# Kernel tuning notes

Hardware: AMD Instinct MI355X
Metric: run time of the kernel (lower is better)

The kernel has to match this reference:

```python
import jax, jax.numpy as jnp
import numpy as np

N, P, C, T, V = 32, 6, 128, 64, 25
S = 3        # num_subset
CI = 32      # inter_channels
EPS = 1e-5
NEG_SLOPE = 0.1


def conv1x1(x, w, b):
    # x: (N,P,Cin,T,V), w: (Cout,Cin), b: (Cout,)
    return jnp.einsum('npctv,oc->npotv', x, w) + b[None, None, :, None, None]


def batchnorm(x, gamma, beta):
    # training-mode BN over (N,P,T,V) per channel, matching torch forward math
    mu = x.mean(axis=(0, 1, 3, 4), keepdims=True)
    var = x.var(axis=(0, 1, 3, 4), keepdims=True)
    xh = (x - mu) * jax.lax.rsqrt(var + EPS)
    return xh * gamma[None, None, :, None, None] + beta[None, None, :, None, None]


def leaky(x):
    return jnp.where(x >= 0, x, NEG_SLOPE * x)


def t_block(inp, att_bias, alphat, w_in, b_in, w_out, b_out, g_out, be_out,
            w_ff, b_ff, g_ff, be_ff):
    n, p, c, t, v = inp.shape
    qk = conv1x1(inp, w_in, b_in)                       # (N,P,2*S*CI,T,V)
    qk = qk.reshape(n, p, 2, S, CI, t, v).transpose(2, 0, 3, 1, 4, 5, 6)
    q, k = qk[0], qk[1]                                 # (N,S,P,CI,T,V)
    scores = jnp.einsum('nspctv,nspcqv->nsptq', q, k) / (CI * v)
    att = att_bias + jnp.tanh(scores) * alphat          # (N,S,P,T,T)
    y = jnp.einsum('npctv,nsptq->nspcqv', inp, att)     # (N,S,P,C,T,V)
    y = y.transpose(0, 2, 1, 3, 4, 5).reshape(n, p, S * c, t, v)
    y = batchnorm(conv1x1(y, w_out, b_out), g_out, be_out)
    y = leaky(inp + y)                                  # residual (identity down path)
    y2 = batchnorm(conv1x1(y, w_ff, b_ff), g_ff, be_ff)
    return leaky(y + y2)


def setup_inputs() -> dict:
    key = jax.random.key(0)
    ks = jax.random.split(key, 8)
    sc = 0.05
    return {
        'x': jax.random.normal(ks[0], (N, P, C, T, V), jnp.float32),
        'att_t1': jnp.zeros((1, S, 1, T, T), jnp.float32),
        'att_t2': jnp.zeros((1, S, 1, T, T), jnp.float32),
        'alphat': jnp.ones((1, S, 1, 1, 1), jnp.float32),
        'w_in': jax.random.normal(ks[1], (2 * S * CI, C), jnp.float32) * sc,
        'b_in': jax.random.normal(ks[2], (2 * S * CI,), jnp.float32) * sc,
        'w_out': jax.random.normal(ks[3], (C, S * C), jnp.float32) * sc,
        'b_out': jax.random.normal(ks[4], (C,), jnp.float32) * sc,
        'g_out': jnp.ones((C,), jnp.float32),
        'be_out': jnp.zeros((C,), jnp.float32),
        'w_ff': jax.random.normal(ks[5], (C, C), jnp.float32) * sc,
        'b_ff': jax.random.normal(ks[6], (C,), jnp.float32) * sc,
        'g_ff': jnp.ones((C,), jnp.float32),
        'be_ff': jnp.zeros((C,), jnp.float32),
    }


def reference(x, att_t1, att_t2, alphat, w_in, b_in, w_out, b_out, g_out,
              be_out, w_ff, b_ff, g_ff, be_ff):
    y = t_block(x, att_t1, alphat, w_in, b_in, w_out, b_out, g_out, be_out,
                w_ff, b_ff, g_ff, be_ff)
    z = t_block(y, att_t2, alphat, w_in, b_in, w_out, b_out, g_out, be_out,
                w_ff, b_ff, g_ff, be_ff)
    return z
```

## Files before the change

kernel.cpp:

```cpp
#include <hip/hip_runtime.h>
#include <hip/hip_bf16.h>
#include <math.h>

#define NPB  192
#define CCH  128
#define TT   64
#define VV   25
#define PIX  1600
#define SS   3
#define EPC  307200.0f
static const size_t ETOT = (size_t)NPB * CCH * PIX;

typedef __attribute__((ext_vector_type(4))) float f32x4;
typedef __attribute__((ext_vector_type(8))) short short8;

__device__ __forceinline__ ushort f2bf(float f) {
    __hip_bfloat16 h = __float2bfloat16(f);
    return __builtin_bit_cast(unsigned short, h);
}
__device__ __forceinline__ float bf2f(ushort u) {
    unsigned int x = ((unsigned int)u) << 16;
    return __builtin_bit_cast(float, x);
}

__global__ void wprep(const float* __restrict__ w_in, const float* __restrict__ b_in,
                      const float* __restrict__ w_out, const float* __restrict__ w_ff,
                      ushort* __restrict__ Wp, float* __restrict__ bp,
                      ushort* __restrict__ Wo, ushort* __restrict__ Wf) {
    int i = blockIdx.x * 256 + threadIdx.x;
    if (i < 192 * 128) {
        int r = i >> 7, c = i & 127;
        int s = r / 64, j = r % 64;
        int src = (j < 32) ? (s * 32 + j) : (96 + s * 32 + (j - 32));
        Wp[i] = f2bf(w_in[src * 128 + c]);
        if (c == 0) bp[r] = b_in[src];
    }
    if (i < 128 * 384) Wo[i] = f2bf(w_out[i]);
    if (i < 128 * 128) Wf[i] = f2bf(w_ff[i]);
}

__global__ void remap_x(const float* __restrict__ x, ushort* __restrict__ xr) {
    size_t o = ((size_t)blockIdx.x * 256 + threadIdx.x) * 4;
    size_t row = o / PIX;
    int p = (int)(o % PIX);
    int v = p >> 6, t0 = p & 63;
    const float* xp = x + row * PIX;
    uint2 u;
    u.x = (uint)f2bf(xp[(t0 + 0) * 25 + v]) | ((uint)f2bf(xp[(t0 + 1) * 25 + v]) << 16);
    u.y = (uint)f2bf(xp[(t0 + 2) * 25 + v]) | ((uint)f2bf(xp[(t0 + 3) * 25 + v]) << 16);
    *(uint2*)(xr + o) = u;
}

__global__ __launch_bounds__(256)
void gemm_conv(const void* __restrict__ inp, int in_bf16,
               const ushort* __restrict__ W, int ldw,
               const float* __restrict__ bias,
               void* __restrict__ outp, int out_bf16, int out_ch,
               int accflag)
{
    __shared__ ushort Wt[64 * 72];
    __shared__ ushort Xt[128 * 72];
    const int np = blockIdx.x;
    const int pixbase = blockIdx.y * 128;
    const int obase = blockIdx.z * 64;
    const int tid = threadIdx.x;
    const int wave = tid >> 6, lane = tid & 63;
    const int quad = lane >> 4, l16 = lane & 15;
    const int wPix = wave * 32;

    f32x4 acc[4][2];
    if (accflag) {
        const float* op = (const float*)outp + ((size_t)np * out_ch + obase) * PIX + pixbase;
#pragma unroll
        for (int ms = 0; ms < 4; ++ms)
#pragma unroll
            for (int ns = 0; ns < 2; ++ns) {
                int pl = wPix + ns * 16 + l16;
                bool valid = (pixbase + pl) < PIX;
#pragma unroll
                for (int r = 0; r < 4; ++r) {
                    int ol = ms * 16 + quad * 4 + r;
                    acc[ms][ns][r] = valid ? op[(size_t)ol * PIX + pl] : 0.f;
                }
            }
    } else {
#pragma unroll
        for (int ms = 0; ms < 4; ++ms) {
            float bv[4];
#pragma unroll
            for (int r = 0; r < 4; ++r) {
                int ol = ms * 16 + quad * 4 + r;
                bv[r] = bias ? bias[obase + ol] : 0.f;
            }
#pragma unroll
            for (int ns = 0; ns < 2; ++ns)
#pragma unroll
                for (int r = 0; r < 4; ++r) acc[ms][ns][r] = bv[r];
        }
    }

    const ushort* inb = (const ushort*)inp;
    const float* inf = (const float*)inp;
    const size_t in_off = (size_t)np * 128 * PIX;

    for (int kc = 0; kc < 2; ++kc) {
        const int kbase = kc * 64;
        {
            int o = tid >> 2, seg = tid & 3;
            const ushort* src = W + (size_t)(obase + o) * ldw + kbase + seg * 16;
            uint4 a = *(const uint4*)src;
            uint4 b = *(const uint4*)(src + 8);
            *(uint4*)&Wt[o * 72 + seg * 16] = a;
            *(uint4*)&Wt[o * 72 + seg * 16 + 8] = b;
        }
        {
            int cp = tid & 31, rq = tid >> 5;
            int c = cp * 2;
            int p0 = rq * 16;
            bool valid = (pixbase + p0) < PIX;
            if (in_bf16) {
                uint ra[8], rb[8];
                if (valid) {
                    const ushort* s0 = inb + in_off + (size_t)(kbase + c) * PIX + pixbase + p0;
                    const ushort* s1 = s0 + PIX;
                    *(uint4*)&ra[0] = *(const uint4*)s0;
                    *(uint4*)&ra[4] = *(const uint4*)(s0 + 8);
                    *(uint4*)&rb[0] = *(const uint4*)s1;
                    *(uint4*)&rb[4] = *(const uint4*)(s1 + 8);
                } else {
#pragma unroll
                    for (int h = 0; h < 8; ++h) { ra[h] = 0; rb[h] = 0; }
                }
#pragma unroll
                for (int h = 0; h < 8; ++h) {
                    uint lo = ra[h], hi = rb[h];
                    *(uint*)&Xt[(p0 + 2 * h) * 72 + c] = (lo & 0xffffu) | (hi << 16);
                    *(uint*)&Xt[(p0 + 2 * h + 1) * 72 + c] = (lo >> 16) | (hi & 0xffff0000u);
                }
            } else {
                if (valid) {
                    const float* s0 = inf + in_off + (size_t)(kbase + c) * PIX + pixbase + p0;
                    const float* s1 = s0 + PIX;
#pragma unroll
                    for (int b4 = 0; b4 < 4; ++b4) {
                        float4 u = ((const float4*)s0)[b4];
                        float4 w4 = ((const float4*)s1)[b4];
                        int p = p0 + b4 * 4;
                        *(uint*)&Xt[(p + 0) * 72 + c] = (uint)f2bf(u.x) | ((uint)f2bf(w4.x) << 16);
                        *(uint*)&Xt[(p + 1) * 72 + c] = (uint)f2bf(u.y) | ((uint)f2bf(w4.y) << 16);
                        *(uint*)&Xt[(p + 2) * 72 + c] = (uint)f2bf(u.z) | ((uint)f2bf(w4.z) << 16);
                        *(uint*)&Xt[(p + 3) * 72 + c] = (uint)f2bf(u.w) | ((uint)f2bf(w4.w) << 16);
                    }
                } else {
#pragma unroll
                    for (int h = 0; h < 16; ++h) *(uint*)&Xt[(p0 + h) * 72 + c] = 0;
                }
            }
        }
        __syncthreads();
#pragma unroll
        for (int ks = 0; ks < 2; ++ks) {
            const int kk = ks * 32;
            short8 a[4], b[2];
#pragma unroll
            for (int ms = 0; ms < 4; ++ms)
                a[ms] = *(const short8*)&Wt[(ms * 16 + l16) * 72 + kk + quad * 8];
#pragma unroll
            for (int ns = 0; ns < 2; ++ns)
                b[ns] = *(const short8*)&Xt[(wPix + ns * 16 + l16) * 72 + kk + quad * 8];
#pragma unroll
            for (int ms = 0; ms < 4; ++ms)
#pragma unroll
                for (int ns = 0; ns < 2; ++ns)
                    acc[ms][ns] = __builtin_amdgcn_mfma_f32_16x16x32_bf16(a[ms], b[ns], acc[ms][ns], 0, 0, 0);
        }
        __syncthreads();
    }

    if (out_bf16) {
        ushort* op = (ushort*)outp + ((size_t)np * out_ch + obase) * PIX + pixbase;
#pragma unroll
        for (int ms = 0; ms < 4; ++ms)
#pragma unroll
            for (int ns = 0; ns < 2; ++ns) {
                int pl = wPix + ns * 16 + l16;
                if (pixbase + pl >= PIX) continue;
#pragma unroll
                for (int r = 0; r < 4; ++r) {
                    int ol = ms * 16 + quad * 4 + r;
                    op[(size_t)ol * PIX + pl] = f2bf(acc[ms][ns][r]);
                }
            }
    } else {
        float* op = (float*)outp + ((size_t)np * out_ch + obase) * PIX + pixbase;
#pragma unroll
        for (int ms = 0; ms < 4; ++ms)
#pragma unroll
            for (int ns = 0; ns < 2; ++ns) {
                int pl = wPix + ns * 16 + l16;
                if (pixbase + pl >= PIX) continue;
#pragma unroll
                for (int r = 0; r < 4; ++r) {
                    int ol = ms * 16 + quad * 4 + r;
                    op[(size_t)ol * PIX + pl] = acc[ms][ns][r];
                }
            }
    }
}

__global__ __launch_bounds__(256)
void scores_mfma(const ushort* __restrict__ qk, const float* __restrict__ attb,
                 const float* __restrict__ alphat, float* __restrict__ att)
{
    __shared__ ushort Qs[64 * 128];
    __shared__ ushort Ks[64 * 128];
    const int np = blockIdx.x, s = blockIdx.y, tid = threadIdx.x;
    const int wave = tid >> 6, lane = tid & 63;
    const int quad = lane >> 4, l16 = lane & 15;
    const int tH = (wave >> 1) * 32, qH = (wave & 1) * 32;
    const ushort* qb = qk + ((size_t)np * 192 + s * 64) * PIX;
    const ushort* kb = qb + (size_t)32 * PIX;

    const int side = wave >> 1;
    const int cil = (wave & 1) * 2 + (lane >> 5);
    const int t0 = (lane & 31) * 2;
    const ushort* sbase = (side ? kb : qb);
    ushort* dst = side ? Ks : Qs;

    f32x4 acc[2][2];
#pragma unroll
    for (int ms = 0; ms < 2; ++ms)
#pragma unroll
        for (int ns = 0; ns < 2; ++ns)
#pragma unroll
            for (int r = 0; r < 4; ++r) acc[ms][ns][r] = 0.f;

    for (int c = 0; c < 8; ++c) {
        __syncthreads();
        {
            const int ci = c * 4 + cil;
            const ushort* sb = sbase + (size_t)ci * PIX + t0;
            uint u[25];
#pragma unroll
            for (int v = 0; v < 25; ++v)
                u[v] = *(const uint*)(sb + v * 64);
            uint rA[16], rB[16];
#pragma unroll
            for (int w2 = 0; w2 < 12; ++w2) {
                uint a = u[2 * w2], b = u[2 * w2 + 1];
                rA[w2] = (a & 0xffffu) | (b << 16);
                rB[w2] = (a >> 16) | (b & 0xffff0000u);
            }
            rA[12] = u[24] & 0xffffu;  rB[12] = u[24] >> 16;
            rA[13] = 0u; rA[14] = 0u; rA[15] = 0u;
            rB[13] = 0u; rB[14] = 0u; rB[15] = 0u;
#pragma unroll
            for (int b4 = 0; b4 < 4; ++b4) {
                int blkA = (cil * 4 + b4) ^ (t0 & 7);
                int blkB = (cil * 4 + b4) ^ ((t0 + 1) & 7);
                uint4 wa, wb;
                wa.x = rA[b4 * 4 + 0]; wa.y = rA[b4 * 4 + 1];
                wa.z = rA[b4 * 4 + 2]; wa.w = rA[b4 * 4 + 3];
                wb.x = rB[b4 * 4 + 0]; wb.y = rB[b4 * 4 + 1];
                wb.z = rB[b4 * 4 + 2]; wb.w = rB[b4 * 4 + 3];
                *(uint4*)&dst[t0 * 128 + blkA * 8] = wa;
                *(uint4*)&dst[(t0 + 1) * 128 + blkB * 8] = wb;
            }
        }
        __syncthreads();
#pragma unroll
        for (int ks = 0; ks < 4; ++ks) {
            short8 a[2], b[2];
#pragma unroll
            for (int ms = 0; ms < 2; ++ms) {
                int t = tH + ms * 16 + l16;
                int blk = (ks * 4 + quad) ^ (t & 7);
                a[ms] = *(const short8*)&Qs[t * 128 + blk * 8];
            }
#pragma unroll
            for (int ns = 0; ns < 2; ++ns) {
                int q = qH + ns * 16 + l16;
                int blk = (ks * 4 + quad) ^ (q & 7);
                b[ns] = *(const short8*)&Ks[q * 128 + blk * 8];
            }
#pragma unroll
            for (int ms = 0; ms < 2; ++ms)
#pragma unroll
                for (int ns = 0; ns < 2; ++ns)
                    acc[ms][ns] = __builtin_amdgcn_mfma_f32_16x16x32_bf16(a[ms], b[ns], acc[ms][ns], 0, 0, 0);
        }
    }

    const float alpha = alphat[s];
    const int n = np / 6, p = np % 6;
    const float* bp2 = attb + (size_t)s * 4096;
    float* ap = att + ((size_t)(n * SS + s) * 6 + p) * 4096;
    const float inv = 1.0f / 800.0f;
#pragma unroll
    for (int ms = 0; ms < 2; ++ms)
#pragma unroll
        for (int ns = 0; ns < 2; ++ns) {
            int q = qH + ns * 16 + l16;
#pragma unroll
            for (int r = 0; r < 4; ++r) {
                int t = tH + ms * 16 + quad * 4 + r;
                ap[t * 64 + q] = bp2[t * 64 + q] + tanhf(acc[ms][ns][r] * inv) * alpha;
            }
        }
}

__global__ __launch_bounds__(256, 4)
void attn_conv(const ushort* __restrict__ xr, const float* __restrict__ att,
               const ushort* __restrict__ Wo, const float* __restrict__ bias,
               float* __restrict__ Z)
{
    __shared__ ushort Xa[128 * 64];
    __shared__ ushort Ta[64 * 64];
    __shared__ ushort Ys[64 * 128];
    const int np = blockIdx.x, v = blockIdx.y, zo = blockIdx.z;
    const int tid = threadIdx.x;
    const int wave = tid >> 6, lane = tid & 63;
    const int quad = lane >> 4, l16 = lane & 15;
    const int mH = (wave & 1) * 64;
    const int oL = (wave & 1) * 32;
    const int qH = (wave >> 1) * 32;
    const int n = np / 6, p = np % 6;

    {
        int cc = tid >> 1, half = tid & 1;
        const ushort* src = xr + ((size_t)np * 128 + cc) * PIX + v * 64 + half * 32;
        uint4 a = *(const uint4*)src;
        uint4 b = *(const uint4*)(src + 8);
        uint4 c0 = *(const uint4*)(src + 16);
        uint4 d = *(const uint4*)(src + 24);
        int sw = cc & 7;
        ushort* xb = &Xa[cc * 64];
        *(uint4*)&xb[((half * 4 + 0) ^ sw) * 8] = a;
        *(uint4*)&xb[((half * 4 + 1) ^ sw) * 8] = b;
        *(uint4*)&xb[((half * 4 + 2) ^ sw) * 8] = c0;
        *(uint4*)&xb[((half * 4 + 3) ^ sw) * 8] = d;
    }

    f32x4 acc2[2][2];
#pragma unroll
    for (int ms2 = 0; ms2 < 2; ++ms2) {
        float bv[4];
#pragma unroll
        for (int r = 0; r < 4; ++r)
            bv[r] = bias[zo * 64 + oL + ms2 * 16 + quad * 4 + r];
#pragma unroll
        for (int ns = 0; ns < 2; ++ns)
#pragma unroll
            for (int r = 0; r < 4; ++r) acc2[ms2][ns][r] = bv[r];
    }

    for (int s = 0; s < SS; ++s) {
        __syncthreads();
        {
            const float* ab = att + ((size_t)(n * SS + s) * 6 + p) * 4096
                              + (size_t)(wave * 16) * 64 + lane;
            ushort tv[16];
#pragma unroll
            for (int i = 0; i < 16; ++i)
                tv[i] = f2bf(ab[i * 64]);
            uint4 wlo, whi;
            wlo.x = (uint)tv[0] | ((uint)tv[1] << 16);
            wlo.y = (uint)tv[2] | ((uint)tv[3] << 16);
            wlo.z = (uint)tv[4] | ((uint)tv[5] << 16);
            wlo.w = (uint)tv[6] | ((uint)tv[7] << 16);
            whi.x = (uint)tv[8] | ((uint)tv[9] << 16);
            whi.y = (uint)tv[10] | ((uint)tv[11] << 16);
            whi.z = (uint)tv[12] | ((uint)tv[13] << 16);
            whi.w = (uint)tv[14] | ((uint)tv[15] << 16);
            int sw = lane & 7;
            ushort* tb = &Ta[lane * 64];
            *(uint4*)&tb[((wave * 2 + 0) ^ sw) * 8] = wlo;
            *(uint4*)&tb[((wave * 2 + 1) ^ sw) * 8] = whi;
        }
        __syncthreads();
        f32x4 acc[4][2];
#pragma unroll
        for (int ms = 0; ms < 4; ++ms)
#pragma unroll
            for (int ns = 0; ns < 2; ++ns)
#pragma unroll
                for (int r = 0; r < 4; ++r) acc[ms][ns][r] = 0.f;
#pragma unroll
        for (int ks = 0; ks < 2; ++ks) {
            short8 a[4], b[2];
#pragma unroll
            for (int ms = 0; ms < 4; ++ms) {
                int row = mH + ms * 16 + l16;
                int blk = (ks * 4 + quad) ^ (l16 & 7);
                a[ms] = *(const short8*)&Xa[row * 64 + blk * 8];
            }
#pragma unroll
            for (int ns = 0; ns < 2; ++ns) {
                int row = qH + ns * 16 + l16;
                int blk = (ks * 4 + quad) ^ (l16 & 7);
                b[ns] = *(const short8*)&Ta[row * 64 + blk * 8];
            }
#pragma unroll
            for (int ms = 0; ms < 4; ++ms)
#pragma unroll
                for (int ns = 0; ns < 2; ++ns)
                    acc[ms][ns] = __builtin_amdgcn_mfma_f32_16x16x32_bf16(a[ms], b[ns], acc[ms][ns], 0, 0, 0);
        }
#pragma unroll
        for (int ms = 0; ms < 4; ++ms)
#pragma unroll
            for (int ns = 0; ns < 2; ++ns) {
                int q = qH + ns * 16 + l16;
                int c0 = mH + ms * 16 + quad * 4;
                uint w0 = (uint)f2bf(acc[ms][ns][0]) | ((uint)f2bf(acc[ms][ns][1]) << 16);
                uint w1 = (uint)f2bf(acc[ms][ns][2]) | ((uint)f2bf(acc[ms][ns][3]) << 16);
                int blk = (c0 >> 3) ^ (q & 7);
                ushort* d = &Ys[q * 128 + blk * 8 + (c0 & 7)];
                *(uint*)d = w0;
                *(uint*)(d + 2) = w1;
            }
        __syncthreads();
        short8 wf[2][4];
        {
            const ushort* wb = Wo + (size_t)(zo * 64 + oL + l16) * 384 + s * 128 + quad * 8;
#pragma unroll
            for (int ms2 = 0; ms2 < 2; ++ms2)
#pragma unroll
                for (int ks2 = 0; ks2 < 4; ++ks2)
                    wf[ms2][ks2] = *(const short8*)(wb + ms2 * 16 * 384 + ks2 * 32);
        }
#pragma unroll
        for (int ks2 = 0; ks2 < 4; ++ks2) {
            short8 b2[2];
#pragma unroll
            for (int ns = 0; ns < 2; ++ns) {
                int q = qH + ns * 16 + l16;
                int blk = (ks2 * 4 + quad) ^ (q & 7);
                b2[ns] = *(const short8*)&Ys[q * 128 + blk * 8];
            }
#pragma unroll
            for (int ms2 = 0; ms2 < 2; ++ms2)
#pragma unroll
                for (int ns = 0; ns < 2; ++ns)
                    acc2[ms2][ns] = __builtin_amdgcn_mfma_f32_16x16x32_bf16(wf[ms2][ks2], b2[ns], acc2[ms2][ns], 0, 0, 0);
        }
    }

    float* zp = Z + ((size_t)np * 128 + zo * 64) * PIX + v * 64;
#pragma unroll
    for (int ms2 = 0; ms2 < 2; ++ms2)
#pragma unroll
        for (int ns = 0; ns < 2; ++ns) {
            int q = qH + ns * 16 + l16;
#pragma unroll
            for (int r = 0; r < 4; ++r) {
                int o = oL + ms2 * 16 + quad * 4 + r;
                zp[(size_t)o * PIX + q] = acc2[ms2][ns][r];
            }
        }
}

__global__ void bn_stats(const float* __restrict__ z, float* __restrict__ stats) {
    const int c = blockIdx.x, np = blockIdx.y, tid = threadIdx.x;
    const float* zp = z + ((size_t)np * CCH + c) * PIX;
    float s = 0.f, s2 = 0.f;
    for (int i = tid; i < PIX; i += 256) {
        float v = zp[i];
        s += v; s2 += v * v;
    }
    for (int off = 32; off; off >>= 1) {
        s += __shfl_down(s, off);
        s2 += __shfl_down(s2, off);
    }
    __shared__ float ls[4], ls2[4];
    const int w = tid >> 6, lane = tid & 63;
    if (lane == 0) { ls[w] = s; ls2[w] = s2; }
    __syncthreads();
    if (tid == 0) {
        s = ls[0] + ls[1] + ls[2] + ls[3];
        s2 = ls2[0] + ls2[1] + ls2[2] + ls2[3];
        atomicAdd(&stats[c], s);
        atomicAdd(&stats[128 + c], s2);
    }
}

__global__ void bn_finalize(const float* __restrict__ stats, const float* __restrict__ g,
                            const float* __restrict__ be, float* __restrict__ scsh) {
    const int c = threadIdx.x;
    float mean = stats[c] * (1.0f / EPC);
    float var = stats[128 + c] * (1.0f / EPC) - mean * mean;
    float inv = rsqrtf(var + 1e-5f);
    float sc = g[c] * inv;
    scsh[c] = sc;
    scsh[128 + c] = be[c] - mean * sc;
}

__global__ void res_bn_g(const float* __restrict__ x, const float* __restrict__ z,
                         const float* __restrict__ scsh, float* __restrict__ out,
                         ushort* __restrict__ outb) {
    size_t i = ((size_t)blockIdx.x * 256 + threadIdx.x) * 4;
    size_t row = i / PIX;
    int p = (int)(i % PIX);
    int ch = (int)(row & 127);
    float sc = scsh[ch], sh = scsh[128 + ch];
    const float* zr = z + row * PIX;
    float4 a = *(const float4*)(x + i);
    float xin[4] = {a.x, a.y, a.z, a.w};
    float4 r;
    float ro[4];
#pragma unroll
    for (int j = 0; j < 4; ++j) {
        int pp = p + j;
        int t = pp / 25, vv = pp - t * 25;
        float zz = zr[vv * 64 + t];
        float val = xin[j] + fmaf(zz, sc, sh);
        ro[j] = val >= 0.f ? val : 0.1f * val;
    }
    r.x = ro[0]; r.y = ro[1]; r.z = ro[2]; r.w = ro[3];
    *(float4*)(out + i) = r;
    uint2 ub;
    ub.x = (uint)f2bf(ro[0]) | ((uint)f2bf(ro[1]) << 16);
    ub.y = (uint)f2bf(ro[2]) | ((uint)f2bf(ro[3]) << 16);
    *(uint2*)(outb + i) = ub;
}

__global__ void res_bn_l(const float4* __restrict__ xr, const float4* __restrict__ zr,
                         const float* __restrict__ scsh, float4* __restrict__ out) {
    int i = blockIdx.x * 256 + threadIdx.x;
    int row = i / 400;
    int ch = row & 127;
    float sc = scsh[ch], sh = scsh[128 + ch];
    float4 a = xr[i], b = zr[i], r;
    r.x = a.x + fmaf(b.x, sc, sh);
    r.y = a.y + fmaf(b.y, sc, sh);
    r.z = a.z + fmaf(b.z, sc, sh);
    r.w = a.w + fmaf(b.w, sc, sh);
    r.x = r.x >= 0.f ? r.x : 0.1f * r.x;
    r.y = r.y >= 0.f ? r.y : 0.1f * r.y;
    r.z = r.z >= 0.f ? r.z : 0.1f * r.z;
    r.w = r.w >= 0.f ? r.w : 0.1f * r.w;
    out[i] = r;
}

struct Ctx {
    ushort *xr, *Wp, *Wo, *Wf;
    float *bp;
    float *R1, *R0, *ATT, *STATS;
    const float *alphat, *b_out, *g_out, *be_out, *b_ff, *g_ff, *be_ff;
};

static void run_block(const float* X, const float* attb, float* OUT,
                      const Ctx& c, hipStream_t stream) {
    const int EG = 38400;
    remap_x<<<EG, 256, 0, stream>>>(X, c.xr);
    gemm_conv<<<dim3(NPB, 13, 3), 256, 0, stream>>>(c.xr, 1, c.Wp, 128, c.bp,
                                                    (void*)c.R1, 1, 192, 0);
    scores_mfma<<<dim3(NPB, 3), 256, 0, stream>>>((const ushort*)c.R1, attb, c.alphat, c.ATT);
    attn_conv<<<dim3(NPB, VV, 2), 256, 0, stream>>>(c.xr, c.ATT, c.Wo, c.b_out, c.R0);
    hipMemsetAsync(c.STATS, 0, 256 * sizeof(float), stream);
    bn_stats<<<dim3(CCH, NPB), 256, 0, stream>>>(c.R0, c.STATS);
    bn_finalize<<<1, 128, 0, stream>>>(c.STATS, c.g_out, c.be_out, c.STATS + 256);
    res_bn_g<<<EG, 256, 0, stream>>>(X, c.R0, c.STATS + 256, c.R1, c.xr);
    gemm_conv<<<dim3(NPB, 13, 2), 256, 0, stream>>>(c.xr, 1, c.Wf, 128, c.b_ff,
                                                    (void*)c.R0, 0, 128, 0);
    hipMemsetAsync(c.STATS, 0, 256 * sizeof(float), stream);
    bn_stats<<<dim3(CCH, NPB), 256, 0, stream>>>(c.R0, c.STATS);
    bn_finalize<<<1, 128, 0, stream>>>(c.STATS, c.g_ff, c.be_ff, c.STATS + 256);
    res_bn_l<<<EG, 256, 0, stream>>>((const float4*)c.R1, (const float4*)c.R0,
                                     c.STATS + 256, (float4*)OUT);
}

extern "C" void kernel_launch(void* const* d_in, const int* in_sizes, int n_in,
                              void* d_out, int out_size, void* d_ws, size_t ws_size,
                              hipStream_t stream) {
    const float* x = (const float*)d_in[0];
    const float* att1 = (const float*)d_in[1];
    const float* att2 = (const float*)d_in[2];
    Ctx c;
    c.alphat = (const float*)d_in[3];
    const float* w_in = (const float*)d_in[4];
    const float* b_in = (const float*)d_in[5];
    const float* w_out = (const float*)d_in[6];
    c.b_out = (const float*)d_in[7];
    c.g_out = (const float*)d_in[8];
    c.be_out = (const float*)d_in[9];
    const float* w_ff = (const float*)d_in[10];
    c.b_ff = (const float*)d_in[11];
    c.g_ff = (const float*)d_in[12];
    c.be_ff = (const float*)d_in[13];

    char* ws = (char*)d_ws;
    size_t off = 0;
    c.xr = (ushort*)(ws + off);   off += ETOT * 2;
    c.R1 = (float*)(ws + off);    off += ETOT * 4;
    c.R0 = (float*)(ws + off);    off += ETOT * 4;
    c.ATT = (float*)(ws + off);   off += (size_t)32 * 3 * 6 * 4096 * 4;
    c.STATS = (float*)(ws + off); off += 512 * 4;
    c.Wp = (ushort*)(ws + off);   off += 192 * 128 * 2;
    c.bp = (float*)(ws + off);    off += 192 * 4;
    c.Wo = (ushort*)(ws + off);   off += 128 * 384 * 2;
    c.Wf = (ushort*)(ws + off);   off += 128 * 128 * 2;

    wprep<<<192, 256, 0, stream>>>(w_in, b_in, w_out, w_ff, c.Wp, c.bp, c.Wo, c.Wf);

    float* out = (float*)d_out;
    run_block(x, att1, out, c, stream);
    run_block(out, att2, out, c, stream);
}
```

Before: 1.583 ms.

## Store attention as transposed bf16 and compute all output channels per attn block

The scores kernel now writes the attention matrix as bf16 in transposed (q,t) layout, so attn_conv can load it with contiguous 16-byte vector loads instead of strided fp32 loads plus conversion. attn_conv drops the z-split over two output-channel halves and each block computes all 128 output channels, so the attention-times-x product is computed once per block rather than twice. The cost is more accumulator registers (8 f32x4 per wave instead of 4) and Wo fragments reloaded per k-step, which may lower occupancy under the 4-blocks launch bound.

```diff
diff --git a/kernel.cpp b/kernel.cpp
--- a/kernel.cpp
+++ b/kernel.cpp
@@ -210,14 +210,14 @@
 
 __global__ __launch_bounds__(256)
 void scores_mfma(const ushort* __restrict__ qk, const float* __restrict__ attb,
-                 const float* __restrict__ alphat, float* __restrict__ att)
+                 const float* __restrict__ alphat, ushort* __restrict__ attq)
 {
     __shared__ ushort Qs[64 * 128];
     __shared__ ushort Ks[64 * 128];
     const int np = blockIdx.x, s = blockIdx.y, tid = threadIdx.x;
     const int wave = tid >> 6, lane = tid & 63;
     const int quad = lane >> 4, l16 = lane & 15;
-    const int tH = (wave >> 1) * 32, qH = (wave & 1) * 32;
+    const int qW = (wave >> 1) * 32, tW = (wave & 1) * 32;
     const ushort* qb = qk + ((size_t)np * 192 + s * 64) * PIX;
     const ushort* kb = qb + (size_t)32 * PIX;
 
@@ -273,15 +273,15 @@
             short8 a[2], b[2];
 #pragma unroll
             for (int ms = 0; ms < 2; ++ms) {
-                int t = tH + ms * 16 + l16;
+                int q = qW + ms * 16 + l16;
+                int blk = (ks * 4 + quad) ^ (q & 7);
+                a[ms] = *(const short8*)&Ks[q * 128 + blk * 8];
+            }
+#pragma unroll
+            for (int ns = 0; ns < 2; ++ns) {
+                int t = tW + ns * 16 + l16;
                 int blk = (ks * 4 + quad) ^ (t & 7);
-                a[ms] = *(const short8*)&Qs[t * 128 + blk * 8];
-            }
-#pragma unroll
-            for (int ns = 0; ns < 2; ++ns) {
-                int q = qH + ns * 16 + l16;
-                int blk = (ks * 4 + quad) ^ (q & 7);
-                b[ns] = *(const short8*)&Ks[q * 128 + blk * 8];
+                b[ns] = *(const short8*)&Qs[t * 128 + blk * 8];
             }
 #pragma unroll
             for (int ms = 0; ms < 2; ++ms)
@@ -294,35 +294,35 @@
     const float alpha = alphat[s];
     const int n = np / 6, p = np % 6;
     const float* bp2 = attb + (size_t)s * 4096;
-    float* ap = att + ((size_t)(n * SS + s) * 6 + p) * 4096;
+    ushort* ap = attq + ((size_t)(n * SS + s) * 6 + p) * 4096;
     const float inv = 1.0f / 800.0f;
 #pragma unroll
     for (int ms = 0; ms < 2; ++ms)
 #pragma unroll
         for (int ns = 0; ns < 2; ++ns) {
-            int q = qH + ns * 16 + l16;
+            int t = tW + ns * 16 + l16;
 #pragma unroll
             for (int r = 0; r < 4; ++r) {
-                int t = tH + ms * 16 + quad * 4 + r;
-                ap[t * 64 + q] = bp2[t * 64 + q] + tanhf(acc[ms][ns][r] * inv) * alpha;
+                int q = qW + ms * 16 + quad * 4 + r;
+                ap[q * 64 + t] = f2bf(bp2[t * 64 + q] + tanhf(acc[ms][ns][r] * inv) * alpha);
             }
         }
 }
 
 __global__ __launch_bounds__(256, 4)
-void attn_conv(const ushort* __restrict__ xr, const float* __restrict__ att,
+void attn_conv(const ushort* __restrict__ xr, const ushort* __restrict__ attq,
                const ushort* __restrict__ Wo, const float* __restrict__ bias,
                float* __restrict__ Z)
 {
     __shared__ ushort Xa[128 * 64];
     __shared__ ushort Ta[64 * 64];
     __shared__ ushort Ys[64 * 128];
-    const int np = blockIdx.x, v = blockIdx.y, zo = blockIdx.z;
+    const int np = blockIdx.x, v = blockIdx.y;
     const int tid = threadIdx.x;
     const int wave = tid >> 6, lane = tid & 63;
     const int quad = lane >> 4, l16 = lane & 15;
     const int mH = (wave & 1) * 64;
-    const int oL = (wave & 1) * 32;
+    const int oH = (wave & 1) * 64;
     const int qH = (wave >> 1) * 32;
     const int n = np / 6, p = np % 6;
 
@@ -341,41 +341,32 @@
         *(uint4*)&xb[((half * 4 + 3) ^ sw) * 8] = d;
     }
 
-    f32x4 acc2[2][2];
-#pragma unroll
-    for (int ms2 = 0; ms2 < 2; ++ms2) {
+    f32x4 acc2[4][2];
+#pragma unroll
+    for (int ms2 = 0; ms2 < 4; ++ms2) {
         float bv[4];
 #pragma unroll
         for (int r = 0; r < 4; ++r)
-            bv[r] = bias[zo * 64 + oL + ms2 * 16 + quad * 4 + r];
+            bv[r] = bias[oH + ms2 * 16 + quad * 4 + r];
 #pragma unroll
         for (int ns = 0; ns < 2; ++ns)
 #pragma unroll
             for (int r = 0; r < 4; ++r) acc2[ms2][ns][r] = bv[r];
     }
 
+    const size_t abase = ((size_t)(n * SS) * 6 + p) * 4096;
+
     for (int s = 0; s < SS; ++s) {
         __syncthreads();
         {
-            const float* ab = att + ((size_t)(n * SS + s) * 6 + p) * 4096
-                              + (size_t)(wave * 16) * 64 + lane;
-            ushort tv[16];
-#pragma unroll
-            for (int i = 0; i < 16; ++i)
-                tv[i] = f2bf(ab[i * 64]);
-            uint4 wlo, whi;
-            wlo.x = (uint)tv[0] | ((uint)tv[1] << 16);
-            wlo.y = (uint)tv[2] | ((uint)tv[3] << 16);
-            wlo.z = (uint)tv[4] | ((uint)tv[5] << 16);
-            wlo.w = (uint)tv[6] | ((uint)tv[7] << 16);
-            whi.x = (uint)tv[8] | ((uint)tv[9] << 16);
-            whi.y = (uint)tv[10] | ((uint)tv[11] << 16);
-            whi.z = (uint)tv[12] | ((uint)tv[13] << 16);
-            whi.w = (uint)tv[14] | ((uint)tv[15] << 16);
-            int sw = lane & 7;
-            ushort* tb = &Ta[lane * 64];
-            *(uint4*)&tb[((wave * 2 + 0) ^ sw) * 8] = wlo;
-            *(uint4*)&tb[((wave * 2 + 1) ^ sw) * 8] = whi;
+            int r0 = tid >> 2, seg = tid & 3;
+            const ushort* src = attq + abase + (size_t)s * 6 * 4096 + r0 * 64 + seg * 16;
+            uint4 a = *(const uint4*)src;
+            uint4 b = *(const uint4*)(src + 8);
+            int sw = r0 & 7;
+            ushort* tb = &Ta[r0 * 64];
+            *(uint4*)&tb[((seg * 2 + 0) ^ sw) * 8] = a;
+            *(uint4*)&tb[((seg * 2 + 1) ^ sw) * 8] = b;
         }
         __syncthreads();
         f32x4 acc[4][2];
@@ -420,17 +411,13 @@
                 *(uint*)(d + 2) = w1;
             }
         __syncthreads();
-        short8 wf[2][4];
-        {
-            const ushort* wb = Wo + (size_t)(zo * 64 + oL + l16) * 384 + s * 128 + quad * 8;
-#pragma unroll
-            for (int ms2 = 0; ms2 < 2; ++ms2)
-#pragma unroll
-                for (int ks2 = 0; ks2 < 4; ++ks2)
-                    wf[ms2][ks2] = *(const short8*)(wb + ms2 * 16 * 384 + ks2 * 32);
-        }
 #pragma unroll
         for (int ks2 = 0; ks2 < 4; ++ks2) {
+            short8 wfa[4];
+            const ushort* wb = Wo + (size_t)(oH + l16) * 384 + s * 128 + ks2 * 32 + quad * 8;
+#pragma unroll
+            for (int ms2 = 0; ms2 < 4; ++ms2)
+                wfa[ms2] = *(const short8*)(wb + (size_t)ms2 * 16 * 384);
             short8 b2[2];
 #pragma unroll
             for (int ns = 0; ns < 2; ++ns) {
@@ -439,22 +426,22 @@
                 b2[ns] = *(const short8*)&Ys[q * 128 + blk * 8];
             }
 #pragma unroll
-            for (int ms2 = 0; ms2 < 2; ++ms2)
+            for (int ms2 = 0; ms2 < 4; ++ms2)
 #pragma unroll
                 for (int ns = 0; ns < 2; ++ns)
-                    acc2[ms2][ns] = __builtin_amdgcn_mfma_f32_16x16x32_bf16(wf[ms2][ks2], b2[ns], acc2[ms2][ns], 0, 0, 0);
-        }
-    }
-
-    float* zp = Z + ((size_t)np * 128 + zo * 64) * PIX + v * 64;
-#pragma unroll
-    for (int ms2 = 0; ms2 < 2; ++ms2)
+                    acc2[ms2][ns] = __builtin_amdgcn_mfma_f32_16x16x32_bf16(wfa[ms2], b2[ns], acc2[ms2][ns], 0, 0, 0);
+        }
+    }
+
+    float* zp = Z + (size_t)np * 128 * PIX + v * 64;
+#pragma unroll
+    for (int ms2 = 0; ms2 < 4; ++ms2)
 #pragma unroll
         for (int ns = 0; ns < 2; ++ns) {
             int q = qH + ns * 16 + l16;
 #pragma unroll
             for (int r = 0; r < 4; ++r) {
-                int o = oL + ms2 * 16 + quad * 4 + r;
+                int o = oH + ms2 * 16 + quad * 4 + r;
                 zp[(size_t)o * PIX + q] = acc2[ms2][ns][r];
             }
         }
@@ -543,9 +530,9 @@
 }
 
 struct Ctx {
-    ushort *xr, *Wp, *Wo, *Wf;
+    ushort *xr, *Wp, *Wo, *Wf, *ATTQ;
     float *bp;
-    float *R1, *R0, *ATT, *STATS;
+    float *R1, *R0, *STATS;
     const float *alphat, *b_out, *g_out, *be_out, *b_ff, *g_ff, *be_ff;
 };
 
@@ -555,8 +542,8 @@
     remap_x<<<EG, 256, 0, stream>>>(X, c.xr);
     gemm_conv<<<dim3(NPB, 13, 3), 256, 0, stream>>>(c.xr, 1, c.Wp, 128, c.bp,
                                                     (void*)c.R1, 1, 192, 0);
-    scores_mfma<<<dim3(NPB, 3), 256, 0, stream>>>((const ushort*)c.R1, attb, c.alphat, c.ATT);
-    attn_conv<<<dim3(NPB, VV, 2), 256, 0, stream>>>(c.xr, c.ATT, c.Wo, c.b_out, c.R0);
+    scores_mfma<<<dim3(NPB, 3), 256, 0, stream>>>((const ushort*)c.R1, attb, c.alphat, c.ATTQ);
+    attn_conv<<<dim3(NPB, VV), 256, 0, stream>>>(c.xr, c.ATTQ, c.Wo, c.b_out, c.R0);
     hipMemsetAsync(c.STATS, 0, 256 * sizeof(float), stream);
     bn_stats<<<dim3(CCH, NPB), 256, 0, stream>>>(c.R0, c.STATS);
     bn_finalize<<<1, 128, 0, stream>>>(c.STATS, c.g_out, c.be_out, c.STATS + 256);
@@ -594,7 +581,7 @@
     c.xr = (ushort*)(ws + off);   off += ETOT * 2;
     c.R1 = (float*)(ws + off);    off += ETOT * 4;
     c.R0 = (float*)(ws + off);    off += ETOT * 4;
-    c.ATT = (float*)(ws + off);   off += (size_t)32 * 3 * 6 * 4096 * 4;
+    c.ATTQ = (ushort*)(ws + off); off += (size_t)32 * 3 * 6 * 4096 * 2;
     c.STATS = (float*)(ws + off); off += 512 * 4;
     c.Wp = (ushort*)(ws + off);   off += 192 * 128 * 2;
     c.bp = (float*)(ws + off);    off += 192 * 4;
```

Result: no change. 1.570 ms (-0.8%).
